# Kernel tuning notes

Measured on AMD Instinct MI355X. Metric: run time of the kernel, lower is better.

The kernel has to match this reference:

```python
import jax, jax.numpy as jnp
import numpy as np

B, T, C = 4, 2048, 2048
H, KV, D = 16, 4, 128          # head_dim = C // H
G = H // KV                     # query heads per kv head
ROPE_BASE = 10000.0


def _rope_tables(T, D, dtype):
    inv_freq = 1.0 / (ROPE_BASE ** (jnp.arange(0, D, 2, dtype=jnp.float32) / D))
    t = jnp.arange(T, dtype=jnp.float32)
    freqs = jnp.outer(t, inv_freq)                 # [T, D/2]
    emb = jnp.concatenate([freqs, freqs], axis=-1) # [T, D]
    return jnp.cos(emb).astype(dtype), jnp.sin(emb).astype(dtype)


def _rotate_half(x):
    x1, x2 = x[..., : x.shape[-1] // 2], x[..., x.shape[-1] // 2 :]
    return jnp.concatenate([-x2, x1], axis=-1)


def setup_inputs() -> dict:
    key = jax.random.key(0)
    ks = jax.random.split(key, 5)
    s = 0.02
    return {
        "x":  jax.random.normal(ks[0], (B, T, C), dtype=jnp.float32),
        "Wq": jax.random.normal(ks[1], (C, H * D), dtype=jnp.float32) * s,
        "Wk": jax.random.normal(ks[2], (C, KV * D), dtype=jnp.float32) * s,
        "Wv": jax.random.normal(ks[3], (C, KV * D), dtype=jnp.float32) * s,
        "Wo": jax.random.normal(ks[4], (C, C), dtype=jnp.float32) * s,
    }


def reference(x, Wq, Wk, Wv, Wo):
    Bc, Tc, Cc = x.shape
    q = (x @ Wq).reshape(Bc, Tc, H, D).transpose(0, 2, 1, 3)   # [B,H,T,D]
    k = (x @ Wk).reshape(Bc, Tc, KV, D).transpose(0, 2, 1, 3)  # [B,KV,T,D]
    v = (x @ Wv).reshape(Bc, Tc, KV, D).transpose(0, 2, 1, 3)  # [B,KV,T,D]

    cos, sin = _rope_tables(Tc, D, x.dtype)                    # [T,D]
    q = q * cos + _rotate_half(q) * sin
    k = k * cos + _rotate_half(k) * sin

    # GQA: broadcast KV heads instead of materializing repeat_interleave.
    # repeat_interleave over head dim == view q as [B,KV,G,T,D] sharing kv head.
    qg = q.reshape(Bc, KV, G, Tc, D)
    scale = D ** -0.5
    scores = jnp.einsum("bkgtd,bksd->bkgts", qg, k) * scale    # [B,KV,G,T,T]
    causal = jnp.tril(jnp.ones((Tc, Tc), dtype=bool))
    scores = jnp.where(causal, scores, jnp.finfo(scores.dtype).min)
    att = jax.nn.softmax(scores, axis=-1)
    out = jnp.einsum("bkgts,bksd->bkgtd", att, v)              # [B,KV,G,T,D]
    out = out.reshape(Bc, H, Tc, D).transpose(0, 2, 1, 3).reshape(Bc, Tc, Cc)
    return out @ Wo
```

## Files before the change

### kernel.cpp

```cpp
#include <hip/hip_runtime.h>
#include <cstdint>

#define DEV __device__ __forceinline__

typedef __attribute__((ext_vector_type(4))) float f32x4;
typedef __attribute__((ext_vector_type(4))) float float4v;
typedef __attribute__((ext_vector_type(8))) short bf16x8;
typedef __attribute__((ext_vector_type(4))) unsigned short ushort4v;
typedef __attribute__((ext_vector_type(2))) unsigned int uint2v;
typedef unsigned short u16;

static constexpr int Bb = 4, Tt = 2048, Hh = 16, KVh = 4, Dd = 128;
static constexpr int NQKV = 3072;

DEV u16 f2bf(float x) {
    union { float f; unsigned u; } v; v.f = x;
    unsigned r = v.u + 0x7FFF + ((v.u >> 16) & 1);
    return (u16)(r >> 16);
}
DEV float bf2f(u16 b) {
    union { unsigned u; float f; } v; v.u = ((unsigned)b) << 16;
    return v.f;
}
DEV unsigned cvtpk(float lo, float hi) {
    unsigned d;
    asm("v_cvt_pk_bf16_f32 %0, %1, %2" : "=v"(d) : "v"(lo), "v"(hi));
    return d;
}

typedef const void __attribute__((address_space(1)))* gas1;
typedef void __attribute__((address_space(3)))* las3;
DEV void gload16(const void* g, void* l) {
    __builtin_amdgcn_global_load_lds((gas1)g, (las3)l, 16, 0, 0);
}

__global__ __launch_bounds__(256) void cast_k(const float* __restrict__ x, u16* __restrict__ xb, long n4) {
    long id = (long)blockIdx.x * 256 + threadIdx.x;
    if (id >= n4) return;
    float4v v = *(const float4v*)&x[id * 4];
    ushort4v o;
    o[0] = f2bf(v[0]); o[1] = f2bf(v[1]); o[2] = f2bf(v[2]); o[3] = f2bf(v[3]);
    *(ushort4v*)&xb[id * 4] = o;
}

__global__ __launch_bounds__(256) void twt_k(const float* __restrict__ W, u16* __restrict__ Wt, int K, int N) {
    __shared__ float tile[32][33];
    int tx = threadIdx.x, ty = threadIdx.y;
    long n0 = (long)blockIdx.x * 32, k0 = (long)blockIdx.y * 32;
#pragma unroll
    for (int j = 0; j < 4; j++)
        tile[ty + j * 8][tx] = W[(k0 + ty + j * 8) * (long)N + n0 + tx];
    __syncthreads();
#pragma unroll
    for (int j = 0; j < 4; j++)
        Wt[(n0 + ty + j * 8) * (long)K + k0 + tx] = f2bf(tile[tx][ty + j * 8]);
}

__global__ __launch_bounds__(256) void tv_k(const u16* __restrict__ qkv, u16* __restrict__ vt) {
    __shared__ u16 tile[32][33];
    int tx = threadIdx.x, ty = threadIdx.y;
    int d0 = blockIdx.x * 32;
    int t0 = blockIdx.y * 32;
    int bk = blockIdx.z;
    int b = bk >> 2, kv = bk & 3;
#pragma unroll
    for (int j = 0; j < 4; j++)
        tile[ty + j * 8][tx] = qkv[(long)(b * Tt + t0 + ty + j * 8) * NQKV + 2560 + kv * Dd + d0 + tx];
    __syncthreads();
#pragma unroll
    for (int j = 0; j < 4; j++)
        vt[((long)(b * KVh + kv) * Dd + d0 + ty + j * 8) * Tt + t0 + tx] = tile[tx][ty + j * 8];
}

__global__ __launch_bounds__(256) void tables_k(float* __restrict__ cosb, float* __restrict__ sinb) {
    int id = blockIdx.x * 256 + threadIdx.x;
    int t = id >> 6, i = id & 63;
    float inv = powf(10000.0f, -(float)i * (1.0f / 64.0f));
    float f = (float)t * inv;
    cosb[id] = cosf(f);
    sinb[id] = sinf(f);
}

__global__ __launch_bounds__(256) void rope_k(u16* __restrict__ p, const float* __restrict__ cosb,
                                              const float* __restrict__ sinb, int nh, float scale, int total,
                                              long rowstride, int colbase) {
    int id = blockIdx.x * 256 + threadIdx.x;
    if (id >= total) return;
    int i = id & 63;
    int bth = id >> 6;
    int row = bth / nh;
    int t = row % Tt;
    u16* ptr = p + (long)row * rowstride + colbase + (bth % nh) * Dd;
    float x1 = bf2f(ptr[i]), x2 = bf2f(ptr[i + 64]);
    float c = cosb[t * 64 + i], s = sinb[t * 64 + i];
    ptr[i] = f2bf((x1 * c - x2 * s) * scale);
    ptr[i + 64] = f2bf((x2 * c + x1 * s) * scale);
}

template <int F32OUT>
__global__ __launch_bounds__(512) void gemm_k(const u16* __restrict__ A, const u16* __restrict__ Bt,
                                              void* __restrict__ Cout, int M, int N, int K) {
    __shared__ u16 lds[3][24576];
    const int tid = threadIdx.x;
    const int lane = tid & 63;
    const int w = __builtin_amdgcn_readfirstlane(tid >> 6);
    const int wm = w >> 1, wn = w & 1;
    const long m0 = (long)blockIdx.x * 256;
    const long n0 = (long)blockIdx.y * 128;
    const int NT = K >> 6;
    const int l8 = lane >> 3, s8 = lane & 7;
    const int fr = lane & 15, kg = lane >> 4;

    auto stageA = [&](int t) {
        u16* base = lds[t % 3];
        const long ko = (long)t * 64;
#pragma unroll
        for (int c4 = 0; c4 < 4; c4++) {
            int c = w * 4 + c4;
            int row = c * 8 + l8;
            int slog = s8 ^ (l8 & 7);
            gload16(A + (m0 + row) * (long)K + ko + slog * 8, base + c * 512);
        }
    };
    auto stageB = [&](int t) {
        u16* base = lds[t % 3];
        const long ko = (long)t * 64;
#pragma unroll
        for (int c2 = 0; c2 < 2; c2++) {
            int c = w * 2 + c2;
            int row = c * 8 + l8;
            int slog = s8 ^ (l8 & 7);
            gload16(Bt + (n0 + row) * (long)K + ko + slog * 8, base + 16384 + c * 512);
        }
    };

    f32x4 acc[4][4] = {};
    stageA(0); stageB(0);
    if (NT > 1) {
        stageA(1); stageB(1);
        asm volatile("s_waitcnt vmcnt(6)" ::: "memory");
    } else {
        asm volatile("s_waitcnt vmcnt(0)" ::: "memory");
    }
    __builtin_amdgcn_s_barrier();

    for (int t = 0; t < NT; ++t) {
        const u16* sa = lds[t % 3];
        const u16* sb = sa + 16384;
        {
            bf16x8 af[4], bfr[4];
#pragma unroll
            for (int i = 0; i < 4; i++) {
                const int row = wm * 64 + i * 16 + fr;
                af[i] = *(const bf16x8*)&sa[row * 64 + ((kg ^ (row & 7)) * 8)];
                const int col = wn * 64 + i * 16 + fr;
                bfr[i] = *(const bf16x8*)&sb[col * 64 + ((kg ^ (col & 7)) * 8)];
            }
            if (t + 2 < NT) stageA(t + 2);
            __builtin_amdgcn_s_barrier();
            __builtin_amdgcn_s_setprio(1);
#pragma unroll
            for (int i = 0; i < 4; i++)
#pragma unroll
                for (int j = 0; j < 4; j++)
                    acc[i][j] = __builtin_amdgcn_mfma_f32_16x16x32_bf16(af[i], bfr[j], acc[i][j], 0, 0, 0);
            __builtin_amdgcn_s_setprio(0);
            __builtin_amdgcn_s_barrier();
        }
        {
            bf16x8 af[4], bfr[4];
#pragma unroll
            for (int i = 0; i < 4; i++) {
                const int row = wm * 64 + i * 16 + fr;
                af[i] = *(const bf16x8*)&sa[row * 64 + (((4 + kg) ^ (row & 7)) * 8)];
                const int col = wn * 64 + i * 16 + fr;
                bfr[i] = *(const bf16x8*)&sb[col * 64 + (((4 + kg) ^ (col & 7)) * 8)];
            }
            if (t + 2 < NT) stageB(t + 2);
            if (t + 2 < NT)
                asm volatile("s_waitcnt vmcnt(6)" ::: "memory");
            else if (t + 1 < NT)
                asm volatile("s_waitcnt vmcnt(0)" ::: "memory");
            __builtin_amdgcn_s_barrier();
            __builtin_amdgcn_s_setprio(1);
#pragma unroll
            for (int i = 0; i < 4; i++)
#pragma unroll
                for (int j = 0; j < 4; j++)
                    acc[i][j] = __builtin_amdgcn_mfma_f32_16x16x32_bf16(af[i], bfr[j], acc[i][j], 0, 0, 0);
            __builtin_amdgcn_s_setprio(0);
            __builtin_amdgcn_s_barrier();
        }
    }

    const int orow = (lane >> 4) * 4, ocol = lane & 15;
#pragma unroll
    for (int i = 0; i < 4; i++)
#pragma unroll
        for (int j = 0; j < 4; j++) {
            long r = m0 + wm * 64 + i * 16 + orow;
            long c = n0 + wn * 64 + j * 16 + ocol;
#pragma unroll
            for (int t = 0; t < 4; t++) {
                if (F32OUT)
                    ((float*)Cout)[(r + t) * N + c] = acc[i][j][t];
                else
                    ((u16*)Cout)[(r + t) * N + c] = f2bf(acc[i][j][t]);
            }
        }
}

__global__ __launch_bounds__(256, 2) void attn_k(const u16* __restrict__ qkv,
                                                 const u16* __restrict__ vt, u16* __restrict__ o) {
    __shared__ u16 kl[2][2][4096];
    __shared__ u16 vl[2][2][4096];
    __shared__ u16 pT[4][16][36];
    const int tid = threadIdx.x;
    const int lane = tid & 63;
    const int w = tid >> 6;
    const int kvb = blockIdx.x;
    const int kv = kvb & 3, b = kvb >> 2;
    const int bid = blockIdx.y;
    const int h = kv * 4 + w;
    const int fr = lane & 15, kg = lane >> 4;
    const long HD = (long)Hh * Dd;
    const long QS = (long)NQKV;
    const long kbase = (long)b * Tt * QS + 2048 + (long)kv * Dd;
    const long vbase = ((long)(b * KVh + kv)) * (long)Dd * Tt;

    auto stage = [&](int bb, int it) {
        const int s0 = it * 64;
        const int lh = lane >> 4;
#pragma unroll
        for (int s = 0; s < 2; s++) {
#pragma unroll
            for (int j = 0; j < 2; j++) {
                int c = j * 4 + w;
                int row = c * 4 + lh;
                int c16 = (lane & 15) ^ (row & 7);
                gload16(qkv + kbase + (long)(s0 + s * 32 + row) * QS + c16 * 8, &kl[bb][s][c * 512]);
            }
#pragma unroll
            for (int j = 0; j < 2; j++) {
                int c = j * 4 + w;
                int rowp = c * 4 + lh;
                int c16u = (lane & 15) ^ (rowp & 7);
                int r = rowp * 4 + (c16u >> 2);
                gload16(vt + vbase + (long)r * Tt + s0 + s * 32 + (c16u & 3) * 8, &vl[bb][s][c * 512]);
            }
        }
    };

    for (int pass = 0; pass < 2; ++pass) {
        const int qt = pass ? bid : 63 - bid;
        const int q0 = qt * 32;
        const long qbase = (long)(b * Tt + q0) * QS + (long)h * Dd;
        const long obase = (long)(b * Tt + q0) * HD + (long)h * Dd;

        bf16x8 qa[2][4];
#pragma unroll
        for (int qi = 0; qi < 2; qi++)
#pragma unroll
            for (int kc = 0; kc < 4; kc++)
                qa[qi][kc] = *(const bf16x8*)&qkv[qbase + (long)(qi * 16 + fr) * QS + kc * 32 + kg * 8];

        f32x4 ot[8][2] = {};
        float mr0 = -1e30f, mr1 = -1e30f, lr0 = 0.0f, lr1 = 0.0f;
        const int nt = (qt + 2) >> 1;

        stage(0, 0);
        __syncthreads();
        int cur = 0;
        for (int it = 0; it < nt; ++it) {
            if (it + 1 < nt) stage(cur ^ 1, it + 1);
            const int s0 = it * 64;
            f32x4 st[4][2] = {};
            __builtin_amdgcn_s_setprio(1);
#pragma unroll
            for (int kf = 0; kf < 4; kf++) {
                const int s = kf >> 1;
                const int rr = (kf & 1) * 16 + fr;
                bf16x8 ka[4];
#pragma unroll
                for (int kc = 0; kc < 4; kc++)
                    ka[kc] = *(const bf16x8*)&kl[cur][s][rr * 128 + (((kc * 4 + kg) ^ (rr & 7)) * 8)];
#pragma unroll
                for (int kc = 0; kc < 4; kc++) {
                    st[kf][0] = __builtin_amdgcn_mfma_f32_16x16x32_bf16(ka[kc], qa[0][kc], st[kf][0], 0, 0, 0);
                    st[kf][1] = __builtin_amdgcn_mfma_f32_16x16x32_bf16(ka[kc], qa[1][kc], st[kf][1], 0, 0, 0);
                }
            }
            __builtin_amdgcn_s_setprio(0);
            if (it == nt - 1) {
#pragma unroll
                for (int kf = 0; kf < 4; kf++)
#pragma unroll
                    for (int qi = 0; qi < 2; qi++) {
                        const int qq = q0 + qi * 16 + fr;
                        const int kb0 = s0 + kf * 16 + kg * 4;
#pragma unroll
                        for (int r = 0; r < 4; r++)
                            if (kb0 + r > qq) st[kf][qi][r] = -1e30f;
                    }
            }
            float tm0 = st[0][0][0], tm1 = st[0][1][0];
#pragma unroll
            for (int kf = 0; kf < 4; kf++)
#pragma unroll
                for (int r = 0; r < 4; r++)
                    if (kf | r) {
                        tm0 = fmaxf(tm0, st[kf][0][r]);
                        tm1 = fmaxf(tm1, st[kf][1][r]);
                    }
            tm0 = fmaxf(tm0, __shfl_xor(tm0, 16)); tm0 = fmaxf(tm0, __shfl_xor(tm0, 32));
            tm1 = fmaxf(tm1, __shfl_xor(tm1, 16)); tm1 = fmaxf(tm1, __shfl_xor(tm1, 32));
            if (__any(fmaxf(tm0 - mr0, tm1 - mr1) > 8.0f)) {
                float mn0 = fmaxf(mr0, tm0), mn1 = fmaxf(mr1, tm1);
                float al0 = __builtin_amdgcn_exp2f(mr0 - mn0);
                float al1 = __builtin_amdgcn_exp2f(mr1 - mn1);
                mr0 = mn0; mr1 = mn1;
                lr0 *= al0; lr1 *= al1;
#pragma unroll
                for (int df = 0; df < 8; df++) { ot[df][0] *= al0; ot[df][1] *= al1; }
            }
            float rs0 = 0.0f, rs1 = 0.0f;
#pragma unroll
            for (int kf = 0; kf < 4; kf++)
#pragma unroll
                for (int r = 0; r < 4; r++) {
                    st[kf][0][r] = __builtin_amdgcn_exp2f(st[kf][0][r] - mr0); rs0 += st[kf][0][r];
                    st[kf][1][r] = __builtin_amdgcn_exp2f(st[kf][1][r] - mr1); rs1 += st[kf][1][r];
                }
            rs0 += __shfl_xor(rs0, 16); rs0 += __shfl_xor(rs0, 32);
            rs1 += __shfl_xor(rs1, 16); rs1 += __shfl_xor(rs1, 32);
            lr0 += rs0; lr1 += rs1;
#pragma unroll
            for (int qi = 0; qi < 2; qi++)
#pragma unroll
                for (int s = 0; s < 2; s++) {
                    uint2v w0;
                    w0[0] = cvtpk(st[2 * s][qi][0], st[2 * s][qi][1]);
                    w0[1] = cvtpk(st[2 * s][qi][2], st[2 * s][qi][3]);
                    *(uint2v*)&pT[w][fr][kg * 4] = w0;
                    uint2v w1;
                    w1[0] = cvtpk(st[2 * s + 1][qi][0], st[2 * s + 1][qi][1]);
                    w1[1] = cvtpk(st[2 * s + 1][qi][2], st[2 * s + 1][qi][3]);
                    *(uint2v*)&pT[w][fr][16 + kg * 4] = w1;
                    bf16x8 bq = *(const bf16x8*)&pT[w][fr][kg * 8];
                    __builtin_amdgcn_s_setprio(1);
#pragma unroll
                    for (int df = 0; df < 8; df++) {
                        const int r = df * 16 + fr;
                        const int rowp = r >> 2;
                        const int c16 = (((r & 3) * 4 + kg) ^ (rowp & 7));
                        bf16x8 va = *(const bf16x8*)&vl[cur][s][rowp * 128 + c16 * 8];
                        ot[df][qi] = __builtin_amdgcn_mfma_f32_16x16x32_bf16(va, bq, ot[df][qi], 0, 0, 0);
                    }
                    __builtin_amdgcn_s_setprio(0);
                }
            __syncthreads();
            cur ^= 1;
        }
        const float il0 = 1.0f / lr0, il1 = 1.0f / lr1;
#pragma unroll
        for (int df = 0; df < 8; df++) {
            uint2v w0, w1;
            w0[0] = cvtpk(ot[df][0][0] * il0, ot[df][0][1] * il0);
            w0[1] = cvtpk(ot[df][0][2] * il0, ot[df][0][3] * il0);
            w1[0] = cvtpk(ot[df][1][0] * il1, ot[df][1][1] * il1);
            w1[1] = cvtpk(ot[df][1][2] * il1, ot[df][1][3] * il1);
            *(uint2v*)&o[obase + (long)(fr) * HD + df * 16 + kg * 4] = w0;
            *(uint2v*)&o[obase + (long)(16 + fr) * HD + df * 16 + kg * 4] = w1;
        }
    }
}

extern "C" void kernel_launch(void* const* d_in, const int* in_sizes, int n_in,
                              void* d_out, int out_size, void* d_ws, size_t ws_size,
                              hipStream_t stream) {
    (void)in_sizes; (void)n_in; (void)out_size; (void)ws_size;
    const float* x = (const float*)d_in[0];
    const float* Wq = (const float*)d_in[1];
    const float* Wk = (const float*)d_in[2];
    const float* Wv = (const float*)d_in[3];
    const float* Wo = (const float*)d_in[4];

    char* ws = (char*)d_ws;
    u16* xb   = (u16*)(ws + 0);
    u16* vtb  = (u16*)(ws + 50331648);
    u16* wqt  = (u16*)(ws + 58720256);
    u16* wkt  = (u16*)(ws + 67108864);
    u16* wvt  = (u16*)(ws + 69206016);
    u16* wot  = (u16*)(ws + 71303168);
    float* cosb = (float*)(ws + 79691776);
    float* sinb = (float*)(ws + 80216064);
    u16* qkv = (u16*)d_out;

    dim3 tb(32, 8);
    cast_k<<<16384, 256, 0, stream>>>(x, xb, 4194304);
    twt_k<<<dim3(64, 64), tb, 0, stream>>>(Wq, wqt, 2048, 2048);
    twt_k<<<dim3(16, 64), tb, 0, stream>>>(Wk, wkt, 2048, 512);
    twt_k<<<dim3(16, 64), tb, 0, stream>>>(Wv, wvt, 2048, 512);
    twt_k<<<dim3(64, 64), tb, 0, stream>>>(Wo, wot, 2048, 2048);
    tables_k<<<512, 256, 0, stream>>>(cosb, sinb);

    gemm_k<0><<<dim3(32, 24), 512, 0, stream>>>(xb, wqt, qkv, 8192, NQKV, 2048);

    rope_k<<<32768, 256, 0, stream>>>(qkv, cosb, sinb, 16, 0.1275174316f, 8388608, NQKV, 0);
    rope_k<<<8192, 256, 0, stream>>>(qkv, cosb, sinb, 4, 1.0f, 2097152, NQKV, 2048);
    tv_k<<<dim3(4, 64, 16), tb, 0, stream>>>(qkv, vtb);

    attn_k<<<dim3(16, 32), 256, 0, stream>>>(qkv, vtb, xb);

    gemm_k<1><<<dim3(32, 16), 512, 0, stream>>>(xb, wot, d_out, 8192, 2048, 2048);
}
```

Measured before the change: 351.5 us.

## Vectorize RoPE and split attention into one q-tile per block with 32-key steps

The RoPE kernel now handles eight elements per thread using vector loads and stores for the activations and the cos/sin tables, which cuts thread count and memory transactions. The attention kernel drops the two-pass pairing of a long and a short q-tile per block. It now launches one block per q-tile (twice the grid), steps through keys in 32-wide tiles instead of 64, halves the LDS staging, and raises occupancy to 3 blocks per CU. The aim is better parallelism and occupancy, at the cost of more loop iterations and barriers per key and a loss of the explicit long/short load balancing.

```diff
diff --git a/kernel.cpp b/kernel.cpp
--- a/kernel.cpp
+++ b/kernel.cpp
@@ -82,19 +82,37 @@
 }
 
 __global__ __launch_bounds__(256) void rope_k(u16* __restrict__ p, const float* __restrict__ cosb,
-                                              const float* __restrict__ sinb, int nh, float scale, int total,
+                                              const float* __restrict__ sinb, int nh, float scale, int total8,
                                               long rowstride, int colbase) {
     int id = blockIdx.x * 256 + threadIdx.x;
-    if (id >= total) return;
-    int i = id & 63;
-    int bth = id >> 6;
+    if (id >= total8) return;
+    int i8 = id & 7;
+    int bth = id >> 3;
     int row = bth / nh;
     int t = row % Tt;
-    u16* ptr = p + (long)row * rowstride + colbase + (bth % nh) * Dd;
-    float x1 = bf2f(ptr[i]), x2 = bf2f(ptr[i + 64]);
-    float c = cosb[t * 64 + i], s = sinb[t * 64 + i];
-    ptr[i] = f2bf((x1 * c - x2 * s) * scale);
-    ptr[i + 64] = f2bf((x2 * c + x1 * s) * scale);
+    u16* ptr = p + (long)row * rowstride + colbase + (bth % nh) * Dd + i8 * 8;
+    ushort4v a0 = *(ushort4v*)&ptr[0];
+    ushort4v a1 = *(ushort4v*)&ptr[4];
+    ushort4v b0 = *(ushort4v*)&ptr[64];
+    ushort4v b1 = *(ushort4v*)&ptr[68];
+    const float4v c0 = *(const float4v*)&cosb[t * 64 + i8 * 8];
+    const float4v c1 = *(const float4v*)&cosb[t * 64 + i8 * 8 + 4];
+    const float4v s0 = *(const float4v*)&sinb[t * 64 + i8 * 8];
+    const float4v s1 = *(const float4v*)&sinb[t * 64 + i8 * 8 + 4];
+    ushort4v oa0, oa1, ob0, ob1;
+#pragma unroll
+    for (int j = 0; j < 4; j++) {
+        float x1 = bf2f(a0[j]), x2 = bf2f(b0[j]);
+        oa0[j] = f2bf((x1 * c0[j] - x2 * s0[j]) * scale);
+        ob0[j] = f2bf((x2 * c0[j] + x1 * s0[j]) * scale);
+        float y1 = bf2f(a1[j]), y2 = bf2f(b1[j]);
+        oa1[j] = f2bf((y1 * c1[j] - y2 * s1[j]) * scale);
+        ob1[j] = f2bf((y2 * c1[j] + y1 * s1[j]) * scale);
+    }
+    *(ushort4v*)&ptr[0] = oa0;
+    *(ushort4v*)&ptr[4] = oa1;
+    *(ushort4v*)&ptr[64] = ob0;
+    *(ushort4v*)&ptr[68] = ob1;
 }
 
 template <int F32OUT>
@@ -210,168 +228,162 @@
         }
 }
 
-__global__ __launch_bounds__(256, 2) void attn_k(const u16* __restrict__ qkv,
+__global__ __launch_bounds__(256, 3) void attn_k(const u16* __restrict__ qkv,
                                                  const u16* __restrict__ vt, u16* __restrict__ o) {
-    __shared__ u16 kl[2][2][4096];
-    __shared__ u16 vl[2][2][4096];
-    __shared__ u16 pT[4][16][36];
+    __shared__ u16 kl[2][4096];
+    __shared__ u16 vl[2][4096];
+    __shared__ u16 pT[4][2][16][36];
     const int tid = threadIdx.x;
     const int lane = tid & 63;
     const int w = tid >> 6;
     const int kvb = blockIdx.x;
     const int kv = kvb & 3, b = kvb >> 2;
-    const int bid = blockIdx.y;
+    const int qt = 63 - (int)blockIdx.y;
+    const int q0 = qt * 32;
     const int h = kv * 4 + w;
     const int fr = lane & 15, kg = lane >> 4;
     const long HD = (long)Hh * Dd;
     const long QS = (long)NQKV;
     const long kbase = (long)b * Tt * QS + 2048 + (long)kv * Dd;
     const long vbase = ((long)(b * KVh + kv)) * (long)Dd * Tt;
+    const long qbase = (long)(b * Tt + q0) * QS + (long)h * Dd;
+    const long obase = (long)(b * Tt + q0) * HD + (long)h * Dd;
 
     auto stage = [&](int bb, int it) {
-        const int s0 = it * 64;
+        const int s0 = it * 32;
         const int lh = lane >> 4;
 #pragma unroll
-        for (int s = 0; s < 2; s++) {
-#pragma unroll
-            for (int j = 0; j < 2; j++) {
-                int c = j * 4 + w;
-                int row = c * 4 + lh;
-                int c16 = (lane & 15) ^ (row & 7);
-                gload16(qkv + kbase + (long)(s0 + s * 32 + row) * QS + c16 * 8, &kl[bb][s][c * 512]);
-            }
-#pragma unroll
-            for (int j = 0; j < 2; j++) {
-                int c = j * 4 + w;
-                int rowp = c * 4 + lh;
-                int c16u = (lane & 15) ^ (rowp & 7);
-                int r = rowp * 4 + (c16u >> 2);
-                gload16(vt + vbase + (long)r * Tt + s0 + s * 32 + (c16u & 3) * 8, &vl[bb][s][c * 512]);
-            }
+        for (int j = 0; j < 2; j++) {
+            int c = j * 4 + w;
+            int row = c * 4 + lh;
+            int c16 = (lane & 15) ^ (row & 7);
+            gload16(qkv + kbase + (long)(s0 + row) * QS + c16 * 8, &kl[bb][c * 512]);
+        }
+#pragma unroll
+        for (int j = 0; j < 2; j++) {
+            int c = j * 4 + w;
+            int rowp = c * 4 + lh;
+            int c16u = (lane & 15) ^ (rowp & 7);
+            int r = rowp * 4 + (c16u >> 2);
+            gload16(vt + vbase + (long)r * Tt + s0 + (c16u & 3) * 8, &vl[bb][c * 512]);
         }
     };
 
-    for (int pass = 0; pass < 2; ++pass) {
-        const int qt = pass ? bid : 63 - bid;
-        const int q0 = qt * 32;
-        const long qbase = (long)(b * Tt + q0) * QS + (long)h * Dd;
-        const long obase = (long)(b * Tt + q0) * HD + (long)h * Dd;
-
-        bf16x8 qa[2][4];
-#pragma unroll
-        for (int qi = 0; qi < 2; qi++)
+    bf16x8 qa[2][4];
+#pragma unroll
+    for (int qi = 0; qi < 2; qi++)
+#pragma unroll
+        for (int kc = 0; kc < 4; kc++)
+            qa[qi][kc] = *(const bf16x8*)&qkv[qbase + (long)(qi * 16 + fr) * QS + kc * 32 + kg * 8];
+
+    f32x4 ot[8][2] = {};
+    float mr0 = -1e30f, mr1 = -1e30f, lr0 = 0.0f, lr1 = 0.0f;
+    const int nt = qt + 1;
+
+    stage(0, 0);
+    __syncthreads();
+    int cur = 0;
+    for (int it = 0; it < nt; ++it) {
+        if (it + 1 < nt) stage(cur ^ 1, it + 1);
+        const int s0 = it * 32;
+        f32x4 st[2][2] = {};
+        __builtin_amdgcn_s_setprio(1);
+#pragma unroll
+        for (int kf = 0; kf < 2; kf++) {
+            const int rr = kf * 16 + fr;
+            bf16x8 ka[4];
 #pragma unroll
             for (int kc = 0; kc < 4; kc++)
-                qa[qi][kc] = *(const bf16x8*)&qkv[qbase + (long)(qi * 16 + fr) * QS + kc * 32 + kg * 8];
-
-        f32x4 ot[8][2] = {};
-        float mr0 = -1e30f, mr1 = -1e30f, lr0 = 0.0f, lr1 = 0.0f;
-        const int nt = (qt + 2) >> 1;
-
-        stage(0, 0);
+                ka[kc] = *(const bf16x8*)&kl[cur][rr * 128 + (((kc * 4 + kg) ^ (rr & 7)) * 8)];
+#pragma unroll
+            for (int kc = 0; kc < 4; kc++) {
+                st[kf][0] = __builtin_amdgcn_mfma_f32_16x16x32_bf16(ka[kc], qa[0][kc], st[kf][0], 0, 0, 0);
+                st[kf][1] = __builtin_amdgcn_mfma_f32_16x16x32_bf16(ka[kc], qa[1][kc], st[kf][1], 0, 0, 0);
+            }
+        }
+        __builtin_amdgcn_s_setprio(0);
+        if (it == nt - 1) {
+#pragma unroll
+            for (int kf = 0; kf < 2; kf++)
+#pragma unroll
+                for (int qi = 0; qi < 2; qi++) {
+                    const int qq = q0 + qi * 16 + fr;
+                    const int kb0 = s0 + kf * 16 + kg * 4;
+#pragma unroll
+                    for (int r = 0; r < 4; r++)
+                        if (kb0 + r > qq) st[kf][qi][r] = -1e30f;
+                }
+        }
+        float tm0 = st[0][0][0], tm1 = st[0][1][0];
+#pragma unroll
+        for (int kf = 0; kf < 2; kf++)
+#pragma unroll
+            for (int r = 0; r < 4; r++)
+                if (kf | r) {
+                    tm0 = fmaxf(tm0, st[kf][0][r]);
+                    tm1 = fmaxf(tm1, st[kf][1][r]);
+                }
+        tm0 = fmaxf(tm0, __shfl_xor(tm0, 16)); tm0 = fmaxf(tm0, __shfl_xor(tm0, 32));
+        tm1 = fmaxf(tm1, __shfl_xor(tm1, 16)); tm1 = fmaxf(tm1, __shfl_xor(tm1, 32));
+        if (__any(fmaxf(tm0 - mr0, tm1 - mr1) > 8.0f)) {
+            float mn0 = fmaxf(mr0, tm0), mn1 = fmaxf(mr1, tm1);
+            float al0 = __builtin_amdgcn_exp2f(mr0 - mn0);
+            float al1 = __builtin_amdgcn_exp2f(mr1 - mn1);
+            mr0 = mn0; mr1 = mn1;
+            lr0 *= al0; lr1 *= al1;
+#pragma unroll
+            for (int df = 0; df < 8; df++) { ot[df][0] *= al0; ot[df][1] *= al1; }
+        }
+        float rs0 = 0.0f, rs1 = 0.0f;
+#pragma unroll
+        for (int kf = 0; kf < 2; kf++)
+#pragma unroll
+            for (int r = 0; r < 4; r++) {
+                st[kf][0][r] = __builtin_amdgcn_exp2f(st[kf][0][r] - mr0); rs0 += st[kf][0][r];
+                st[kf][1][r] = __builtin_amdgcn_exp2f(st[kf][1][r] - mr1); rs1 += st[kf][1][r];
+            }
+        rs0 += __shfl_xor(rs0, 16); rs0 += __shfl_xor(rs0, 32);
+        rs1 += __shfl_xor(rs1, 16); rs1 += __shfl_xor(rs1, 32);
+        lr0 += rs0; lr1 += rs1;
+#pragma unroll
+        for (int qi = 0; qi < 2; qi++) {
+            uint2v w0;
+            w0[0] = cvtpk(st[0][qi][0], st[0][qi][1]);
+            w0[1] = cvtpk(st[0][qi][2], st[0][qi][3]);
+            *(uint2v*)&pT[w][qi][fr][kg * 4] = w0;
+            uint2v w1;
+            w1[0] = cvtpk(st[1][qi][0], st[1][qi][1]);
+            w1[1] = cvtpk(st[1][qi][2], st[1][qi][3]);
+            *(uint2v*)&pT[w][qi][fr][16 + kg * 4] = w1;
+        }
+        {
+            bf16x8 bq0 = *(const bf16x8*)&pT[w][0][fr][kg * 8];
+            bf16x8 bq1 = *(const bf16x8*)&pT[w][1][fr][kg * 8];
+            __builtin_amdgcn_s_setprio(1);
+#pragma unroll
+            for (int df = 0; df < 8; df++) {
+                const int r = df * 16 + fr;
+                const int rowp = r >> 2;
+                const int c16 = (((r & 3) * 4 + kg) ^ (rowp & 7));
+                bf16x8 va = *(const bf16x8*)&vl[cur][rowp * 128 + c16 * 8];
+                ot[df][0] = __builtin_amdgcn_mfma_f32_16x16x32_bf16(va, bq0, ot[df][0], 0, 0, 0);
+                ot[df][1] = __builtin_amdgcn_mfma_f32_16x16x32_bf16(va, bq1, ot[df][1], 0, 0, 0);
+            }
+            __builtin_amdgcn_s_setprio(0);
+        }
         __syncthreads();
-        int cur = 0;
-        for (int it = 0; it < nt; ++it) {
-            if (it + 1 < nt) stage(cur ^ 1, it + 1);
-            const int s0 = it * 64;
-            f32x4 st[4][2] = {};
-            __builtin_amdgcn_s_setprio(1);
-#pragma unroll
-            for (int kf = 0; kf < 4; kf++) {
-                const int s = kf >> 1;
-                const int rr = (kf & 1) * 16 + fr;
-                bf16x8 ka[4];
-#pragma unroll
-                for (int kc = 0; kc < 4; kc++)
-                    ka[kc] = *(const bf16x8*)&kl[cur][s][rr * 128 + (((kc * 4 + kg) ^ (rr & 7)) * 8)];
-#pragma unroll
-                for (int kc = 0; kc < 4; kc++) {
-                    st[kf][0] = __builtin_amdgcn_mfma_f32_16x16x32_bf16(ka[kc], qa[0][kc], st[kf][0], 0, 0, 0);
-                    st[kf][1] = __builtin_amdgcn_mfma_f32_16x16x32_bf16(ka[kc], qa[1][kc], st[kf][1], 0, 0, 0);
-                }
-            }
-            __builtin_amdgcn_s_setprio(0);
-            if (it == nt - 1) {
-#pragma unroll
-                for (int kf = 0; kf < 4; kf++)
-#pragma unroll
-                    for (int qi = 0; qi < 2; qi++) {
-                        const int qq = q0 + qi * 16 + fr;
-                        const int kb0 = s0 + kf * 16 + kg * 4;
-#pragma unroll
-                        for (int r = 0; r < 4; r++)
-                            if (kb0 + r > qq) st[kf][qi][r] = -1e30f;
-                    }
-            }
-            float tm0 = st[0][0][0], tm1 = st[0][1][0];
-#pragma unroll
-            for (int kf = 0; kf < 4; kf++)
-#pragma unroll
-                for (int r = 0; r < 4; r++)
-                    if (kf | r) {
-                        tm0 = fmaxf(tm0, st[kf][0][r]);
-                        tm1 = fmaxf(tm1, st[kf][1][r]);
-                    }
-            tm0 = fmaxf(tm0, __shfl_xor(tm0, 16)); tm0 = fmaxf(tm0, __shfl_xor(tm0, 32));
-            tm1 = fmaxf(tm1, __shfl_xor(tm1, 16)); tm1 = fmaxf(tm1, __shfl_xor(tm1, 32));
-            if (__any(fmaxf(tm0 - mr0, tm1 - mr1) > 8.0f)) {
-                float mn0 = fmaxf(mr0, tm0), mn1 = fmaxf(mr1, tm1);
-                float al0 = __builtin_amdgcn_exp2f(mr0 - mn0);
-                float al1 = __builtin_amdgcn_exp2f(mr1 - mn1);
-                mr0 = mn0; mr1 = mn1;
-                lr0 *= al0; lr1 *= al1;
-#pragma unroll
-                for (int df = 0; df < 8; df++) { ot[df][0] *= al0; ot[df][1] *= al1; }
-            }
-            float rs0 = 0.0f, rs1 = 0.0f;
-#pragma unroll
-            for (int kf = 0; kf < 4; kf++)
-#pragma unroll
-                for (int r = 0; r < 4; r++) {
-                    st[kf][0][r] = __builtin_amdgcn_exp2f(st[kf][0][r] - mr0); rs0 += st[kf][0][r];
-                    st[kf][1][r] = __builtin_amdgcn_exp2f(st[kf][1][r] - mr1); rs1 += st[kf][1][r];
-                }
-            rs0 += __shfl_xor(rs0, 16); rs0 += __shfl_xor(rs0, 32);
-            rs1 += __shfl_xor(rs1, 16); rs1 += __shfl_xor(rs1, 32);
-            lr0 += rs0; lr1 += rs1;
-#pragma unroll
-            for (int qi = 0; qi < 2; qi++)
-#pragma unroll
-                for (int s = 0; s < 2; s++) {
-                    uint2v w0;
-                    w0[0] = cvtpk(st[2 * s][qi][0], st[2 * s][qi][1]);
-                    w0[1] = cvtpk(st[2 * s][qi][2], st[2 * s][qi][3]);
-                    *(uint2v*)&pT[w][fr][kg * 4] = w0;
-                    uint2v w1;
-                    w1[0] = cvtpk(st[2 * s + 1][qi][0], st[2 * s + 1][qi][1]);
-                    w1[1] = cvtpk(st[2 * s + 1][qi][2], st[2 * s + 1][qi][3]);
-                    *(uint2v*)&pT[w][fr][16 + kg * 4] = w1;
-                    bf16x8 bq = *(const bf16x8*)&pT[w][fr][kg * 8];
-                    __builtin_amdgcn_s_setprio(1);
-#pragma unroll
-                    for (int df = 0; df < 8; df++) {
-                        const int r = df * 16 + fr;
-                        const int rowp = r >> 2;
-                        const int c16 = (((r & 3) * 4 + kg) ^ (rowp & 7));
-                        bf16x8 va = *(const bf16x8*)&vl[cur][s][rowp * 128 + c16 * 8];
-                        ot[df][qi] = __builtin_amdgcn_mfma_f32_16x16x32_bf16(va, bq, ot[df][qi], 0, 0, 0);
-                    }
-                    __builtin_amdgcn_s_setprio(0);
-                }
-            __syncthreads();
-            cur ^= 1;
-        }
-        const float il0 = 1.0f / lr0, il1 = 1.0f / lr1;
-#pragma unroll
-        for (int df = 0; df < 8; df++) {
-            uint2v w0, w1;
-            w0[0] = cvtpk(ot[df][0][0] * il0, ot[df][0][1] * il0);
-            w0[1] = cvtpk(ot[df][0][2] * il0, ot[df][0][3] * il0);
-            w1[0] = cvtpk(ot[df][1][0] * il1, ot[df][1][1] * il1);
-            w1[1] = cvtpk(ot[df][1][2] * il1, ot[df][1][3] * il1);
-            *(uint2v*)&o[obase + (long)(fr) * HD + df * 16 + kg * 4] = w0;
-            *(uint2v*)&o[obase + (long)(16 + fr) * HD + df * 16 + kg * 4] = w1;
-        }
+        cur ^= 1;
+    }
+    const float il0 = 1.0f / lr0, il1 = 1.0f / lr1;
+#pragma unroll
+    for (int df = 0; df < 8; df++) {
+        uint2v w0, w1;
+        w0[0] = cvtpk(ot[df][0][0] * il0, ot[df][0][1] * il0);
+        w0[1] = cvtpk(ot[df][0][2] * il0, ot[df][0][3] * il0);
+        w1[0] = cvtpk(ot[df][1][0] * il1, ot[df][1][1] * il1);
+        w1[1] = cvtpk(ot[df][1][2] * il1, ot[df][1][3] * il1);
+        *(uint2v*)&o[obase + (long)(fr) * HD + df * 16 + kg * 4] = w0;
+        *(uint2v*)&o[obase + (long)(16 + fr) * HD + df * 16 + kg * 4] = w1;
     }
 }
 
@@ -406,11 +418,11 @@
 
     gemm_k<0><<<dim3(32, 24), 512, 0, stream>>>(xb, wqt, qkv, 8192, NQKV, 2048);
 
-    rope_k<<<32768, 256, 0, stream>>>(qkv, cosb, sinb, 16, 0.1275174316f, 8388608, NQKV, 0);
-    rope_k<<<8192, 256, 0, stream>>>(qkv, cosb, sinb, 4, 1.0f, 2097152, NQKV, 2048);
+    rope_k<<<4096, 256, 0, stream>>>(qkv, cosb, sinb, 16, 0.1275174316f, 1048576, NQKV, 0);
+    rope_k<<<1024, 256, 0, stream>>>(qkv, cosb, sinb, 4, 1.0f, 262144, NQKV, 2048);
     tv_k<<<dim3(4, 64, 16), tb, 0, stream>>>(qkv, vtb);
 
-    attn_k<<<dim3(16, 32), 256, 0, stream>>>(qkv, vtb, xb);
+    attn_k<<<dim3(16, 64), 256, 0, stream>>>(qkv, vtb, xb);
 
     gemm_k<1><<<dim3(32, 16), 512, 0, stream>>>(xb, wot, d_out, 8192, 2048, 2048);
 }
```

Result: faster. 344.5 us (-2.0%).
